# Performance work log

Measured on AMD Instinct MI355X. Metric: run time of the kernel, lower is better.

## Reference

```python
import jax, jax.numpy as jnp
import numpy as np

T, B, D, H = 512, 256, 256, 256


def setup_inputs() -> dict:
    key = jax.random.key(0)
    ks = jax.random.split(key, 10)
    # ragged lengths in [T//2, T], sorted descending as pack_padded_sequence requires
    lengths = np.sort(np.random.RandomState(0).randint(T // 2, T + 1, size=B))[::-1]
    # batch_sizes[t] = number of sequences still active at step t (non-increasing, >=1)
    batch_sizes = (lengths[None, :] > np.arange(T)[:, None]).sum(axis=1).astype(np.int32)
    batch_sizes = np.maximum(batch_sizes, 1)
    return {
        "input_x": jax.random.normal(ks[0], (T, B, D), jnp.float32),
        "h0": jax.random.normal(ks[1], (B, H), jnp.float32),
        "c0": jax.random.normal(ks[2], (B, H), jnp.float32),
        # variational dropout masks (precomputed, applied multiplicatively every step)
        "mask_x": (jax.random.uniform(ks[3], (B, D)) > 0.3).astype(jnp.float32) / 0.7,
        "mask_h": (jax.random.uniform(ks[4], (B, H)) > 0.3).astype(jnp.float32) / 0.7,
        "W_ih": jax.random.normal(ks[5], (4 * H, D), jnp.float32) * 0.05,
        "W_hh": jax.random.normal(ks[6], (4 * H, H), jnp.float32) * 0.05,
        "b_ih": jax.random.normal(ks[7], (4 * H,), jnp.float32) * 0.05,
        "b_hh": jax.random.normal(ks[8], (4 * H,), jnp.float32) * 0.05,
        "batch_sizes": jnp.asarray(batch_sizes),
    }


def reference(input_x, h0, c0, mask_x, mask_h, W_ih, W_hh, b_ih, b_hh, batch_sizes):
    # Forward (is_reversed=False) variational-dropout LSTM over a packed sequence.
    # Packed data is kept padded [T,B,*]; batch_sizes gives active rows per step.
    # Inactive rows keep their last-active hidden/cell state (== hn semantics).
    Bsz, Hid = h0.shape
    row = jnp.arange(Bsz)[:, None]

    def step(carry, inp):
        h, c = carry
        x_t, size = inp
        active = row < size  # [B,1]
        xi = x_t * mask_x            # input variational dropout
        hi = h * mask_h              # hidden variational dropout
        gates = xi @ W_ih.T + b_ih + hi @ W_hh.T + b_hh  # [B, 4H]
        i, f, g, o = jnp.split(gates, 4, axis=-1)
        c_new = jax.nn.sigmoid(f) * c + jax.nn.sigmoid(i) * jnp.tanh(g)
        h_new = jax.nn.sigmoid(o) * jnp.tanh(c_new)
        h = jnp.where(active, h_new, h)
        c = jnp.where(active, c_new, c)
        out = jnp.where(active, h_new, 0.0)  # padded positions zeroed (unused in pack)
        return (h, c), out

    (hn, cn), output = jax.lax.scan(step, (h0, c0), (input_x, batch_sizes))
    return output, hn, cn
```

## Files before the change

### kernel.cpp

```cpp
#include <hip/hip_runtime.h>
#include <hip/hip_bf16.h>

#define T_STEPS 512
#define BATCH   256
#define DIM     256
#define HID     256
#define DEPTH   4

using bf16x8  = __attribute__((ext_vector_type(8))) __bf16;
using floatx4 = __attribute__((ext_vector_type(4))) float;
typedef unsigned long long u64;
typedef unsigned int u32;

__device__ __forceinline__ float sigf(float x)   { return 1.0f / (1.0f + __expf(-x)); }
__device__ __forceinline__ float tanh_f(float x) { return 1.0f - 2.0f / (1.0f + __expf(2.0f * x)); }

__device__ __forceinline__ bf16x8 cvt8(const float* p) {
  floatx4 a = *(const floatx4*)p;
  floatx4 b = *(const floatx4*)(p + 4);
  bf16x8 r;
  r[0]=(__bf16)a[0]; r[1]=(__bf16)a[1]; r[2]=(__bf16)a[2]; r[3]=(__bf16)a[3];
  r[4]=(__bf16)b[0]; r[5]=(__bf16)b[1]; r[6]=(__bf16)b[2]; r[7]=(__bf16)b[3];
  return r;
}
__device__ __forceinline__ u32 f2bf(float f) {
  union { float f; u32 u; } v; v.f = f;
  u32 lsb = (v.u >> 16) & 1;
  return (v.u + 0x7fff + lsb) >> 16;
}
__device__ __forceinline__ float bf2f(u32 u) {
  union { u32 u; float f; } v; v.u = u << 16; return v.f;
}

__global__ void init_ws(int* __restrict__ flg, u64* __restrict__ inbox) {
  const int idx = blockIdx.x * 256 + threadIdx.x;
  if (idx < 4096) flg[idx] = 0;
  if (idx < 65536) inbox[idx] = 0ull;
}

__global__ __launch_bounds__(512, 1) void lstm_pk3(
    const float* __restrict__ x, const float* __restrict__ h0,
    const float* __restrict__ c0,
    const float* __restrict__ mask_x, const float* __restrict__ mask_h,
    const float* __restrict__ W_ih, const float* __restrict__ W_hh,
    const float* __restrict__ b_ih, const float* __restrict__ b_hh,
    const int* __restrict__ bs_g,
    float* __restrict__ out, float* __restrict__ hn_out, float* __restrict__ cn_out,
    int* __restrict__ flg, float* __restrict__ ring, u64* __restrict__ inbox) {

  const int tid  = threadIdx.x;
  const int g    = blockIdx.x & 15;
  const int role = blockIdx.x >> 4;
  const int p    = role & 1;
  const int row_base = g * 16;
  const int lane = tid & 63;
  const int w    = tid >> 6;
  const int l15  = lane & 15;
  const int l4   = lane >> 4;

  __shared__ alignas(16) __bf16 s_ab[16 * 256];
  __shared__ int s_bs[T_STEPS];
  for (int i = tid; i < T_STEPS; i += 512) s_bs[i] = bs_g[i];
  __syncthreads();

  int* cons_flg_mine = flg + (g * 2 + p) * 32;
  int* prod_flg_mine = flg + 2048 + (g * 2 + p) * 32;
  float* ring_mine = ring + (size_t)(g * 2 + p) * (DEPTH * 8192);
  u64* inbox_mine    = inbox + (size_t)(g * 2 + p) * 2048;
  u64* inbox_partner = inbox + (size_t)(g * 2 + (1 - p)) * 2048;

  const int c_loc = w * 16 + l15;

  if (role >= 2) {
    bf16x8 wih_r[4][8];
    #pragma unroll
    for (int q = 0; q < 4; ++q) {
      const size_t wr = (size_t)(q * HID + p * 128 + c_loc) * DIM;
      #pragma unroll
      for (int m = 0; m < 8; ++m) wih_r[q][m] = cvt8(W_ih + wr + m * 32 + l4 * 8);
    }
    float bias[4];
    #pragma unroll
    for (int q = 0; q < 4; ++q) {
      const int bc = q * HID + p * 128 + c_loc;
      bias[q] = b_ih[bc] + b_hh[bc];
    }
    const int srow = tid & 15, scb = (tid >> 4) * 8;
    floatx4 mx0 = *(const floatx4*)(mask_x + (row_base + srow) * DIM + scb);
    floatx4 mx1 = *(const floatx4*)(mask_x + (row_base + srow) * DIM + scb + 4);
    const int soff = (srow * 512 + scb * 2) ^ ((srow & 7) << 4);

    for (int t = 0; t < T_STEPS; ++t) {
      if (s_bs[t] <= row_base) break;
      if (t >= DEPTH) {
        const int tgt = t - (DEPTH - 1);
        while (__hip_atomic_load(cons_flg_mine, __ATOMIC_RELAXED, __HIP_MEMORY_SCOPE_AGENT) < tgt) {}
      }
      const float* xp = x + ((size_t)t * BATCH + row_base + srow) * DIM + scb;
      floatx4 xa = *(const floatx4*)xp;
      floatx4 xb = *(const floatx4*)(xp + 4);
      bf16x8 xv;
      #pragma unroll
      for (int e = 0; e < 4; ++e) { xv[e] = (__bf16)(xa[e] * mx0[e]); xv[4 + e] = (__bf16)(xb[e] * mx1[e]); }
      *(bf16x8*)((char*)s_ab + soff) = xv;
      asm volatile("s_waitcnt lgkmcnt(0)" ::: "memory");
      __builtin_amdgcn_s_barrier();

      floatx4 a0, a1, a2, a3;
      a0 = a1 = a2 = a3 = (floatx4)(0.0f);
      #pragma unroll
      for (int m = 0; m < 8; ++m) {
        const int ab = (l15 * 512 + l4 * 16 + m * 64) ^ ((l15 & 7) << 4);
        bf16x8 ax = *(const bf16x8*)((const char*)s_ab + ab);
        a0 = __builtin_amdgcn_mfma_f32_16x16x32_bf16(ax, wih_r[0][m], a0, 0, 0, 0);
        a1 = __builtin_amdgcn_mfma_f32_16x16x32_bf16(ax, wih_r[1][m], a1, 0, 0, 0);
        a2 = __builtin_amdgcn_mfma_f32_16x16x32_bf16(ax, wih_r[2][m], a2, 0, 0, 0);
        a3 = __builtin_amdgcn_mfma_f32_16x16x32_bf16(ax, wih_r[3][m], a3, 0, 0, 0);
      }
      float* rs = ring_mine + (size_t)(t & (DEPTH - 1)) * 8192;
      #pragma unroll
      for (int e = 0; e < 4; ++e) {
        const int rb = (l4 * 4 + e) * 4;
        __hip_atomic_store(rs + (rb + 0) * 128 + c_loc, a0[e] + bias[0], __ATOMIC_RELAXED, __HIP_MEMORY_SCOPE_AGENT);
        __hip_atomic_store(rs + (rb + 1) * 128 + c_loc, a1[e] + bias[1], __ATOMIC_RELAXED, __HIP_MEMORY_SCOPE_AGENT);
        __hip_atomic_store(rs + (rb + 2) * 128 + c_loc, a2[e] + bias[2], __ATOMIC_RELAXED, __HIP_MEMORY_SCOPE_AGENT);
        __hip_atomic_store(rs + (rb + 3) * 128 + c_loc, a3[e] + bias[3], __ATOMIC_RELAXED, __HIP_MEMORY_SCOPE_AGENT);
      }
      asm volatile("s_waitcnt vmcnt(0)" ::: "memory");
      __builtin_amdgcn_s_barrier();
      if (tid == 0)
        __hip_atomic_store(prod_flg_mine, t + 1, __ATOMIC_RELAXED, __HIP_MEMORY_SCOPE_AGENT);
    }
    return;
  }

  const int c_own = p * 128 + c_loc;
  bf16x8 whh_r[4][8];
  #pragma unroll
  for (int q = 0; q < 4; ++q) {
    const size_t wr = (size_t)(q * HID + c_own) * HID;
    const float* wown = W_hh + wr + p * 128;
    const float* wpar = W_hh + wr + (1 - p) * 128;
    #pragma unroll
    for (int i = 0; i < 4; ++i) {
      whh_r[q][i]     = cvt8(wown + i * 32 + l4 * 8);
      whh_r[q][4 + i] = cvt8(wpar + i * 32 + l4 * 8);
    }
  }
  float mh_c[4], h_[4], c_[4];
  #pragma unroll
  for (int e = 0; e < 4; ++e) {
    const int grow = row_base + l4 * 4 + e;
    mh_c[e] = mask_h[grow * HID + c_own];
    h_[e]   = h0[grow * HID + c_own];
    c_[e]   = c0[grow * HID + c_own];
  }
  const int sc_loc = tid >> 2;
  const int rq     = tid & 3;
  const int c_gs   = (1 - p) * 128 + sc_loc;
  float mh_s[4];
  #pragma unroll
  for (int e = 0; e < 4; ++e) mh_s[e] = mask_h[(row_base + rq * 4 + e) * HID + c_gs];

  const int abase   = l15 * 512 + l4 * 16;
  const int own_off = p * 256;
  const int par_off = (1 - p) * 256;

  #pragma unroll
  for (int e = 0; e < 4; ++e) {
    const int r = l4 * 4 + e;
    const int off = (r * 512 + c_own * 2) ^ ((r & 7) << 4);
    *(__bf16*)((char*)s_ab + off) = (__bf16)(h_[e] * mh_c[e]);
  }
  while (__hip_atomic_load(prod_flg_mine, __ATOMIC_RELAXED, __HIP_MEMORY_SCOPE_AGENT) < 1) {}
  asm volatile("" ::: "memory");
  float xp_c[16];
  #pragma unroll
  for (int e = 0; e < 4; ++e)
    #pragma unroll
    for (int q = 0; q < 4; ++q)
      xp_c[e * 4 + q] = __hip_atomic_load(ring_mine + ((l4 * 4 + e) * 4 + q) * 128 + c_loc,
                                          __ATOMIC_RELAXED, __HIP_MEMORY_SCOPE_AGENT);
  asm volatile("s_waitcnt lgkmcnt(0)" ::: "memory");
  __builtin_amdgcn_s_barrier();

  for (int t = 0; t < T_STEPS; ++t) {
    const int bszt = s_bs[t];
    if (bszt <= row_base) {
      #pragma unroll
      for (int e = 0; e < 4; ++e)
        out[(size_t)t * (BATCH * HID) + (row_base + l4 * 4 + e) * HID + c_own] = 0.0f;
      continue;
    }
    const bool act_n = (t + 1 < T_STEPS) && (s_bs[t + 1] > row_base);

    floatx4 a0, a1, a2, a3;
    a0 = a1 = a2 = a3 = (floatx4)(0.0f);
    #pragma unroll
    for (int i = 0; i < 4; ++i) {
      const int ab = ((abase + own_off + i * 64)) ^ ((l15 & 7) << 4);
      bf16x8 ah = *(const bf16x8*)((const char*)s_ab + ab);
      a0 = __builtin_amdgcn_mfma_f32_16x16x32_bf16(ah, whh_r[0][i], a0, 0, 0, 0);
      a1 = __builtin_amdgcn_mfma_f32_16x16x32_bf16(ah, whh_r[1][i], a1, 0, 0, 0);
      a2 = __builtin_amdgcn_mfma_f32_16x16x32_bf16(ah, whh_r[2][i], a2, 0, 0, 0);
      a3 = __builtin_amdgcn_mfma_f32_16x16x32_bf16(ah, whh_r[3][i], a3, 0, 0, 0);
    }

    if (t == 0) {
      #pragma unroll
      for (int e = 0; e < 4; ++e) {
        const int r = rq * 4 + e;
        const float hv = h0[(row_base + r) * HID + c_gs] * mh_s[e];
        const int off = (r * 512 + c_gs * 2) ^ ((r & 7) << 4);
        *(__bf16*)((char*)s_ab + off) = (__bf16)hv;
      }
    } else {
      const u64* ib = inbox_mine + (size_t)(t & 1) * 1024 + sc_loc * 8 + rq * 2;
      u64 pk0, pk1;
      do {
        pk0 = __hip_atomic_load(ib,     __ATOMIC_RELAXED, __HIP_MEMORY_SCOPE_AGENT);
        pk1 = __hip_atomic_load(ib + 1, __ATOMIC_RELAXED, __HIP_MEMORY_SCOPE_AGENT);
      } while (!__all((int)(((u32)pk0 == (u32)t) && ((u32)pk1 == (u32)t))));
      float hv[4];
      hv[0] = bf2f((u32)(pk0 >> 32) & 0xffffu) * mh_s[0];
      hv[1] = bf2f((u32)(pk0 >> 48))           * mh_s[1];
      hv[2] = bf2f((u32)(pk1 >> 32) & 0xffffu) * mh_s[2];
      hv[3] = bf2f((u32)(pk1 >> 48))           * mh_s[3];
      #pragma unroll
      for (int e = 0; e < 4; ++e) {
        const int r = rq * 4 + e;
        const int off = (r * 512 + c_gs * 2) ^ ((r & 7) << 4);
        *(__bf16*)((char*)s_ab + off) = (__bf16)hv[e];
      }
    }
    asm volatile("s_waitcnt lgkmcnt(0)" ::: "memory");
    __builtin_amdgcn_s_barrier();

    #pragma unroll
    for (int i = 0; i < 4; ++i) {
      const int ab = ((abase + par_off + i * 64)) ^ ((l15 & 7) << 4);
      bf16x8 ah = *(const bf16x8*)((const char*)s_ab + ab);
      a0 = __builtin_amdgcn_mfma_f32_16x16x32_bf16(ah, whh_r[0][4 + i], a0, 0, 0, 0);
      a1 = __builtin_amdgcn_mfma_f32_16x16x32_bf16(ah, whh_r[1][4 + i], a1, 0, 0, 0);
      a2 = __builtin_amdgcn_mfma_f32_16x16x32_bf16(ah, whh_r[2][4 + i], a2, 0, 0, 0);
      a3 = __builtin_amdgcn_mfma_f32_16x16x32_bf16(ah, whh_r[3][4 + i], a3, 0, 0, 0);
    }

    float o_[4];
    #pragma unroll
    for (int e = 0; e < 4; ++e) {
      const bool ract = (row_base + l4 * 4 + e) < bszt;
      const float iv = sigf(a0[e] + xp_c[e * 4 + 0]);
      const float fv = sigf(a1[e] + xp_c[e * 4 + 1]);
      const float gv = tanh_f(a2[e] + xp_c[e * 4 + 2]);
      const float ov = sigf(a3[e] + xp_c[e * 4 + 3]);
      const float cc = fv * c_[e] + iv * gv;
      const float hh = ov * tanh_f(cc);
      if (ract) { c_[e] = cc; h_[e] = hh; }
      o_[e] = ract ? hh : 0.0f;
    }

    if (act_n) {
      u64* ob = inbox_partner + (size_t)((t + 1) & 1) * 1024 + c_loc * 8 + l4 * 2;
      const u64 tag = (u32)(t + 1);
      u64 w0 = tag | ((u64)f2bf(h_[0]) << 32) | ((u64)f2bf(h_[1]) << 48);
      u64 w1 = tag | ((u64)f2bf(h_[2]) << 32) | ((u64)f2bf(h_[3]) << 48);
      __hip_atomic_store(ob,     w0, __ATOMIC_RELAXED, __HIP_MEMORY_SCOPE_AGENT);
      __hip_atomic_store(ob + 1, w1, __ATOMIC_RELAXED, __HIP_MEMORY_SCOPE_AGENT);
    }

    if (act_n) {
      #pragma unroll
      for (int e = 0; e < 4; ++e) {
        const int r = l4 * 4 + e;
        const int off = (r * 512 + c_own * 2) ^ ((r & 7) << 4);
        *(__bf16*)((char*)s_ab + off) = (__bf16)(h_[e] * mh_c[e]);
      }
    }
    #pragma unroll
    for (int e = 0; e < 4; ++e)
      out[(size_t)t * (BATCH * HID) + (row_base + l4 * 4 + e) * HID + c_own] = o_[e];

    if (act_n) {
      if (tid == 0)
        __hip_atomic_store(cons_flg_mine, t + 1, __ATOMIC_RELAXED, __HIP_MEMORY_SCOPE_AGENT);
      while (__hip_atomic_load(prod_flg_mine, __ATOMIC_RELAXED, __HIP_MEMORY_SCOPE_AGENT) < t + 2) {}
      asm volatile("" ::: "memory");
      const float* rs = ring_mine + (size_t)((t + 1) & (DEPTH - 1)) * 8192;
      #pragma unroll
      for (int e = 0; e < 4; ++e)
        #pragma unroll
        for (int q = 0; q < 4; ++q)
          xp_c[e * 4 + q] = __hip_atomic_load(rs + ((l4 * 4 + e) * 4 + q) * 128 + c_loc,
                                              __ATOMIC_RELAXED, __HIP_MEMORY_SCOPE_AGENT);
    }

    asm volatile("s_waitcnt lgkmcnt(0)" ::: "memory");
    __builtin_amdgcn_s_barrier();
  }

  #pragma unroll
  for (int e = 0; e < 4; ++e) {
    const int grow = row_base + l4 * 4 + e;
    hn_out[grow * HID + c_own] = h_[e];
    cn_out[grow * HID + c_own] = c_[e];
  }
}

extern "C" void kernel_launch(void* const* d_in, const int* in_sizes, int n_in,
                              void* d_out, int out_size, void* d_ws, size_t ws_size,
                              hipStream_t stream) {
  const float* x      = (const float*)d_in[0];
  const float* h0     = (const float*)d_in[1];
  const float* c0     = (const float*)d_in[2];
  const float* mask_x = (const float*)d_in[3];
  const float* mask_h = (const float*)d_in[4];
  const float* W_ih   = (const float*)d_in[5];
  const float* W_hh   = (const float*)d_in[6];
  const float* b_ih   = (const float*)d_in[7];
  const float* b_hh   = (const float*)d_in[8];
  const int*   bs     = (const int*)d_in[9];

  float* out = (float*)d_out;
  float* hn  = out + (size_t)T_STEPS * BATCH * HID;
  float* cn  = hn + (size_t)BATCH * HID;

  int* flg  = (int*)d_ws;
  float* ring = (float*)((char*)d_ws + 16384);
  u64* inbox = (u64*)((char*)d_ws + 16384 + 4194304);

  init_ws<<<256, 256, 0, stream>>>(flg, inbox);
  lstm_pk3<<<64, 512, 0, stream>>>(x, h0, c0, mask_x, mask_h, W_ih, W_hh,
                                   b_ih, b_hh, bs, out, hn, cn, flg, ring, inbox);
}
```

Before: 1.640 ms.

## Tag ring entries in bf16 and batch output stores through shared memory

The producer now writes the input-projection ring as tagged u64 words holding packed bf16 values. Consumers spin on the tags directly, so the separate producer flag, its vmcnt wait and the flag store go away, and ring traffic is halved. The next step's x is prefetched during the MFMAs, and per-step outputs are staged in shared memory and flushed every 8 steps. The trade-offs are lower precision for the projection values, stale tags that may match across calls because the ring and inbox are no longer zeroed, and more shared memory use.

```diff
diff --git a/kernel.cpp b/kernel.cpp
--- a/kernel.cpp
+++ b/kernel.cpp
@@ -29,16 +29,14 @@
   return (v.u + 0x7fff + lsb) >> 16;
 }
 __device__ __forceinline__ float bf2f(u32 u) {
-  union { u32 u; float f; } v; v.u = u << 16; return v.f;
-}
-
-__global__ void init_ws(int* __restrict__ flg, u64* __restrict__ inbox) {
-  const int idx = blockIdx.x * 256 + threadIdx.x;
-  if (idx < 4096) flg[idx] = 0;
-  if (idx < 65536) inbox[idx] = 0ull;
-}
-
-__global__ __launch_bounds__(512, 1) void lstm_pk3(
+  union { u32 u; float f; } v; v.u = (u & 0xffffu) << 16; return v.f;
+}
+
+__global__ void init_ws(int* __restrict__ flg) {
+  flg[blockIdx.x * 256 + threadIdx.x] = 0;
+}
+
+__global__ __launch_bounds__(512, 1) void lstm_v9(
     const float* __restrict__ x, const float* __restrict__ h0,
     const float* __restrict__ c0,
     const float* __restrict__ mask_x, const float* __restrict__ mask_h,
@@ -46,7 +44,7 @@
     const float* __restrict__ b_ih, const float* __restrict__ b_hh,
     const int* __restrict__ bs_g,
     float* __restrict__ out, float* __restrict__ hn_out, float* __restrict__ cn_out,
-    int* __restrict__ flg, float* __restrict__ ring, u64* __restrict__ inbox) {
+    int* __restrict__ flg, u64* __restrict__ ring, u64* __restrict__ inbox) {
 
   const int tid  = threadIdx.x;
   const int g    = blockIdx.x & 15;
@@ -59,13 +57,13 @@
   const int l4   = lane >> 4;
 
   __shared__ alignas(16) __bf16 s_ab[16 * 256];
+  __shared__ alignas(16) float  s_ob[512 * 32];
   __shared__ int s_bs[T_STEPS];
   for (int i = tid; i < T_STEPS; i += 512) s_bs[i] = bs_g[i];
   __syncthreads();
 
   int* cons_flg_mine = flg + (g * 2 + p) * 32;
-  int* prod_flg_mine = flg + 2048 + (g * 2 + p) * 32;
-  float* ring_mine = ring + (size_t)(g * 2 + p) * (DEPTH * 8192);
+  u64* ring_mine     = ring + (size_t)(g * 2 + p) * (DEPTH * 4096);
   u64* inbox_mine    = inbox + (size_t)(g * 2 + p) * 2048;
   u64* inbox_partner = inbox + (size_t)(g * 2 + (1 - p)) * 2048;
 
@@ -89,6 +87,12 @@
     floatx4 mx0 = *(const floatx4*)(mask_x + (row_base + srow) * DIM + scb);
     floatx4 mx1 = *(const floatx4*)(mask_x + (row_base + srow) * DIM + scb + 4);
     const int soff = (srow * 512 + scb * 2) ^ ((srow & 7) << 4);
+
+    floatx4 xa, xb;
+    {
+      const float* xp = x + (size_t)(row_base + srow) * DIM + scb;
+      xa = *(const floatx4*)xp; xb = *(const floatx4*)(xp + 4);
+    }
 
     for (int t = 0; t < T_STEPS; ++t) {
       if (s_bs[t] <= row_base) break;
@@ -96,9 +100,6 @@
         const int tgt = t - (DEPTH - 1);
         while (__hip_atomic_load(cons_flg_mine, __ATOMIC_RELAXED, __HIP_MEMORY_SCOPE_AGENT) < tgt) {}
       }
-      const float* xp = x + ((size_t)t * BATCH + row_base + srow) * DIM + scb;
-      floatx4 xa = *(const floatx4*)xp;
-      floatx4 xb = *(const floatx4*)(xp + 4);
       bf16x8 xv;
       #pragma unroll
       for (int e = 0; e < 4; ++e) { xv[e] = (__bf16)(xa[e] * mx0[e]); xv[4 + e] = (__bf16)(xb[e] * mx1[e]); }
@@ -117,19 +118,22 @@
         a2 = __builtin_amdgcn_mfma_f32_16x16x32_bf16(ax, wih_r[2][m], a2, 0, 0, 0);
         a3 = __builtin_amdgcn_mfma_f32_16x16x32_bf16(ax, wih_r[3][m], a3, 0, 0, 0);
       }
-      float* rs = ring_mine + (size_t)(t & (DEPTH - 1)) * 8192;
+
+      if (t + 1 < T_STEPS) {
+        const float* xp = x + ((size_t)(t + 1) * BATCH + row_base + srow) * DIM + scb;
+        xa = *(const floatx4*)xp; xb = *(const floatx4*)(xp + 4);
+      }
+
+      u64* rs = ring_mine + (size_t)(t & (DEPTH - 1)) * 4096 + tid * 8;
+      const u64 tag = (u32)(t + 1);
       #pragma unroll
       for (int e = 0; e < 4; ++e) {
-        const int rb = (l4 * 4 + e) * 4;
-        __hip_atomic_store(rs + (rb + 0) * 128 + c_loc, a0[e] + bias[0], __ATOMIC_RELAXED, __HIP_MEMORY_SCOPE_AGENT);
-        __hip_atomic_store(rs + (rb + 1) * 128 + c_loc, a1[e] + bias[1], __ATOMIC_RELAXED, __HIP_MEMORY_SCOPE_AGENT);
-        __hip_atomic_store(rs + (rb + 2) * 128 + c_loc, a2[e] + bias[2], __ATOMIC_RELAXED, __HIP_MEMORY_SCOPE_AGENT);
-        __hip_atomic_store(rs + (rb + 3) * 128 + c_loc, a3[e] + bias[3], __ATOMIC_RELAXED, __HIP_MEMORY_SCOPE_AGENT);
-      }
-      asm volatile("s_waitcnt vmcnt(0)" ::: "memory");
+        u64 w0 = tag | ((u64)f2bf(a0[e] + bias[0]) << 32) | ((u64)f2bf(a1[e] + bias[1]) << 48);
+        u64 w1 = tag | ((u64)f2bf(a2[e] + bias[2]) << 32) | ((u64)f2bf(a3[e] + bias[3]) << 48);
+        __hip_atomic_store(rs + e * 2,     w0, __ATOMIC_RELAXED, __HIP_MEMORY_SCOPE_AGENT);
+        __hip_atomic_store(rs + e * 2 + 1, w1, __ATOMIC_RELAXED, __HIP_MEMORY_SCOPE_AGENT);
+      }
       __builtin_amdgcn_s_barrier();
-      if (tid == 0)
-        __hip_atomic_store(prod_flg_mine, t + 1, __ATOMIC_RELAXED, __HIP_MEMORY_SCOPE_AGENT);
     }
     return;
   }
@@ -172,24 +176,44 @@
     const int off = (r * 512 + c_own * 2) ^ ((r & 7) << 4);
     *(__bf16*)((char*)s_ab + off) = (__bf16)(h_[e] * mh_c[e]);
   }
-  while (__hip_atomic_load(prod_flg_mine, __ATOMIC_RELAXED, __HIP_MEMORY_SCOPE_AGENT) < 1) {}
-  asm volatile("" ::: "memory");
   float xp_c[16];
-  #pragma unroll
-  for (int e = 0; e < 4; ++e)
-    #pragma unroll
-    for (int q = 0; q < 4; ++q)
-      xp_c[e * 4 + q] = __hip_atomic_load(ring_mine + ((l4 * 4 + e) * 4 + q) * 128 + c_loc,
-                                          __ATOMIC_RELAXED, __HIP_MEMORY_SCOPE_AGENT);
+  {
+    const u64* rp = ring_mine + tid * 8;
+    u64 q0,q1,q2,q3,q4,q5,q6,q7;
+    do {
+      q0 = __hip_atomic_load(rp+0, __ATOMIC_RELAXED, __HIP_MEMORY_SCOPE_AGENT);
+      q1 = __hip_atomic_load(rp+1, __ATOMIC_RELAXED, __HIP_MEMORY_SCOPE_AGENT);
+      q2 = __hip_atomic_load(rp+2, __ATOMIC_RELAXED, __HIP_MEMORY_SCOPE_AGENT);
+      q3 = __hip_atomic_load(rp+3, __ATOMIC_RELAXED, __HIP_MEMORY_SCOPE_AGENT);
+      q4 = __hip_atomic_load(rp+4, __ATOMIC_RELAXED, __HIP_MEMORY_SCOPE_AGENT);
+      q5 = __hip_atomic_load(rp+5, __ATOMIC_RELAXED, __HIP_MEMORY_SCOPE_AGENT);
+      q6 = __hip_atomic_load(rp+6, __ATOMIC_RELAXED, __HIP_MEMORY_SCOPE_AGENT);
+      q7 = __hip_atomic_load(rp+7, __ATOMIC_RELAXED, __HIP_MEMORY_SCOPE_AGENT);
+    } while (!__all((int)(((u32)q0==1u)&&((u32)q1==1u)&&((u32)q2==1u)&&((u32)q3==1u)&&
+                          ((u32)q4==1u)&&((u32)q5==1u)&&((u32)q6==1u)&&((u32)q7==1u))));
+    xp_c[0]=bf2f((u32)(q0>>32)); xp_c[1]=bf2f((u32)(q0>>48)); xp_c[2]=bf2f((u32)(q1>>32)); xp_c[3]=bf2f((u32)(q1>>48));
+    xp_c[4]=bf2f((u32)(q2>>32)); xp_c[5]=bf2f((u32)(q2>>48)); xp_c[6]=bf2f((u32)(q3>>32)); xp_c[7]=bf2f((u32)(q3>>48));
+    xp_c[8]=bf2f((u32)(q4>>32)); xp_c[9]=bf2f((u32)(q4>>48)); xp_c[10]=bf2f((u32)(q5>>32)); xp_c[11]=bf2f((u32)(q5>>48));
+    xp_c[12]=bf2f((u32)(q6>>32)); xp_c[13]=bf2f((u32)(q6>>48)); xp_c[14]=bf2f((u32)(q7>>32)); xp_c[15]=bf2f((u32)(q7>>48));
+  }
   asm volatile("s_waitcnt lgkmcnt(0)" ::: "memory");
   __builtin_amdgcn_s_barrier();
 
   for (int t = 0; t < T_STEPS; ++t) {
     const int bszt = s_bs[t];
     if (bszt <= row_base) {
-      #pragma unroll
-      for (int e = 0; e < 4; ++e)
-        out[(size_t)t * (BATCH * HID) + (row_base + l4 * 4 + e) * HID + c_own] = 0.0f;
+      floatx4 z; z[0]=z[1]=z[2]=z[3]=0.0f;
+      *(floatx4*)&s_ob[tid * 32 + (t & 7) * 4] = z;
+      if ((t & 7) == 7) {
+        const int t0 = t - 7;
+        #pragma unroll
+        for (int k = 0; k < 8; ++k) {
+          floatx4 v = *(const floatx4*)&s_ob[tid * 32 + k * 4];
+          #pragma unroll
+          for (int e = 0; e < 4; ++e)
+            out[(size_t)(t0 + k) * (BATCH * HID) + (row_base + l4 * 4 + e) * HID + c_own] = v[e];
+        }
+      }
       continue;
     }
     const bool act_n = (t + 1 < T_STEPS) && (s_bs[t + 1] > row_base);
@@ -198,7 +222,7 @@
     a0 = a1 = a2 = a3 = (floatx4)(0.0f);
     #pragma unroll
     for (int i = 0; i < 4; ++i) {
-      const int ab = ((abase + own_off + i * 64)) ^ ((l15 & 7) << 4);
+      const int ab = (abase + own_off + i * 64) ^ ((l15 & 7) << 4);
       bf16x8 ah = *(const bf16x8*)((const char*)s_ab + ab);
       a0 = __builtin_amdgcn_mfma_f32_16x16x32_bf16(ah, whh_r[0][i], a0, 0, 0, 0);
       a1 = __builtin_amdgcn_mfma_f32_16x16x32_bf16(ah, whh_r[1][i], a1, 0, 0, 0);
@@ -222,10 +246,10 @@
         pk1 = __hip_atomic_load(ib + 1, __ATOMIC_RELAXED, __HIP_MEMORY_SCOPE_AGENT);
       } while (!__all((int)(((u32)pk0 == (u32)t) && ((u32)pk1 == (u32)t))));
       float hv[4];
-      hv[0] = bf2f((u32)(pk0 >> 32) & 0xffffu) * mh_s[0];
-      hv[1] = bf2f((u32)(pk0 >> 48))           * mh_s[1];
-      hv[2] = bf2f((u32)(pk1 >> 32) & 0xffffu) * mh_s[2];
-      hv[3] = bf2f((u32)(pk1 >> 48))           * mh_s[3];
+      hv[0] = bf2f((u32)(pk0 >> 32)) * mh_s[0];
+      hv[1] = bf2f((u32)(pk0 >> 48)) * mh_s[1];
+      hv[2] = bf2f((u32)(pk1 >> 32)) * mh_s[2];
+      hv[3] = bf2f((u32)(pk1 >> 48)) * mh_s[3];
       #pragma unroll
       for (int e = 0; e < 4; ++e) {
         const int r = rq * 4 + e;
@@ -238,7 +262,7 @@
 
     #pragma unroll
     for (int i = 0; i < 4; ++i) {
-      const int ab = ((abase + par_off + i * 64)) ^ ((l15 & 7) << 4);
+      const int ab = (abase + par_off + i * 64) ^ ((l15 & 7) << 4);
       bf16x8 ah = *(const bf16x8*)((const char*)s_ab + ab);
       a0 = __builtin_amdgcn_mfma_f32_16x16x32_bf16(ah, whh_r[0][4 + i], a0, 0, 0, 0);
       a1 = __builtin_amdgcn_mfma_f32_16x16x32_bf16(ah, whh_r[1][4 + i], a1, 0, 0, 0);
@@ -246,7 +270,7 @@
       a3 = __builtin_amdgcn_mfma_f32_16x16x32_bf16(ah, whh_r[3][4 + i], a3, 0, 0, 0);
     }
 
-    float o_[4];
+    floatx4 o4;
     #pragma unroll
     for (int e = 0; e < 4; ++e) {
       const bool ract = (row_base + l4 * 4 + e) < bszt;
@@ -257,7 +281,7 @@
       const float cc = fv * c_[e] + iv * gv;
       const float hh = ov * tanh_f(cc);
       if (ract) { c_[e] = cc; h_[e] = hh; }
-      o_[e] = ract ? hh : 0.0f;
+      o4[e] = ract ? hh : 0.0f;
     }
 
     if (act_n) {
@@ -277,22 +301,39 @@
         *(__bf16*)((char*)s_ab + off) = (__bf16)(h_[e] * mh_c[e]);
       }
     }
-    #pragma unroll
-    for (int e = 0; e < 4; ++e)
-      out[(size_t)t * (BATCH * HID) + (row_base + l4 * 4 + e) * HID + c_own] = o_[e];
+    *(floatx4*)&s_ob[tid * 32 + (t & 7) * 4] = o4;
+    if ((t & 7) == 7) {
+      const int t0 = t - 7;
+      #pragma unroll
+      for (int k = 0; k < 8; ++k) {
+        floatx4 v = *(const floatx4*)&s_ob[tid * 32 + k * 4];
+        #pragma unroll
+        for (int e = 0; e < 4; ++e)
+          out[(size_t)(t0 + k) * (BATCH * HID) + (row_base + l4 * 4 + e) * HID + c_own] = v[e];
+      }
+    }
 
     if (act_n) {
       if (tid == 0)
         __hip_atomic_store(cons_flg_mine, t + 1, __ATOMIC_RELAXED, __HIP_MEMORY_SCOPE_AGENT);
-      while (__hip_atomic_load(prod_flg_mine, __ATOMIC_RELAXED, __HIP_MEMORY_SCOPE_AGENT) < t + 2) {}
-      asm volatile("" ::: "memory");
-      const float* rs = ring_mine + (size_t)((t + 1) & (DEPTH - 1)) * 8192;
-      #pragma unroll
-      for (int e = 0; e < 4; ++e)
-        #pragma unroll
-        for (int q = 0; q < 4; ++q)
-          xp_c[e * 4 + q] = __hip_atomic_load(rs + ((l4 * 4 + e) * 4 + q) * 128 + c_loc,
-                                              __ATOMIC_RELAXED, __HIP_MEMORY_SCOPE_AGENT);
+      const u64* rp = ring_mine + (size_t)((t + 1) & (DEPTH - 1)) * 4096 + tid * 8;
+      const u32 tg = (u32)(t + 2);
+      u64 q0,q1,q2,q3,q4,q5,q6,q7;
+      do {
+        q0 = __hip_atomic_load(rp+0, __ATOMIC_RELAXED, __HIP_MEMORY_SCOPE_AGENT);
+        q1 = __hip_atomic_load(rp+1, __ATOMIC_RELAXED, __HIP_MEMORY_SCOPE_AGENT);
+        q2 = __hip_atomic_load(rp+2, __ATOMIC_RELAXED, __HIP_MEMORY_SCOPE_AGENT);
+        q3 = __hip_atomic_load(rp+3, __ATOMIC_RELAXED, __HIP_MEMORY_SCOPE_AGENT);
+        q4 = __hip_atomic_load(rp+4, __ATOMIC_RELAXED, __HIP_MEMORY_SCOPE_AGENT);
+        q5 = __hip_atomic_load(rp+5, __ATOMIC_RELAXED, __HIP_MEMORY_SCOPE_AGENT);
+        q6 = __hip_atomic_load(rp+6, __ATOMIC_RELAXED, __HIP_MEMORY_SCOPE_AGENT);
+        q7 = __hip_atomic_load(rp+7, __ATOMIC_RELAXED, __HIP_MEMORY_SCOPE_AGENT);
+      } while (!__all((int)(((u32)q0==tg)&&((u32)q1==tg)&&((u32)q2==tg)&&((u32)q3==tg)&&
+                            ((u32)q4==tg)&&((u32)q5==tg)&&((u32)q6==tg)&&((u32)q7==tg))));
+      xp_c[0]=bf2f((u32)(q0>>32)); xp_c[1]=bf2f((u32)(q0>>48)); xp_c[2]=bf2f((u32)(q1>>32)); xp_c[3]=bf2f((u32)(q1>>48));
+      xp_c[4]=bf2f((u32)(q2>>32)); xp_c[5]=bf2f((u32)(q2>>48)); xp_c[6]=bf2f((u32)(q3>>32)); xp_c[7]=bf2f((u32)(q3>>48));
+      xp_c[8]=bf2f((u32)(q4>>32)); xp_c[9]=bf2f((u32)(q4>>48)); xp_c[10]=bf2f((u32)(q5>>32)); xp_c[11]=bf2f((u32)(q5>>48));
+      xp_c[12]=bf2f((u32)(q6>>32)); xp_c[13]=bf2f((u32)(q6>>48)); xp_c[14]=bf2f((u32)(q7>>32)); xp_c[15]=bf2f((u32)(q7>>48));
     }
 
     asm volatile("s_waitcnt lgkmcnt(0)" ::: "memory");
@@ -326,10 +367,10 @@
   float* cn  = hn + (size_t)BATCH * HID;
 
   int* flg  = (int*)d_ws;
-  float* ring = (float*)((char*)d_ws + 16384);
+  u64* ring = (u64*)((char*)d_ws + 16384);
   u64* inbox = (u64*)((char*)d_ws + 16384 + 4194304);
 
-  init_ws<<<256, 256, 0, stream>>>(flg, inbox);
-  lstm_pk3<<<64, 512, 0, stream>>>(x, h0, c0, mask_x, mask_h, W_ih, W_hh,
-                                   b_ih, b_hh, bs, out, hn, cn, flg, ring, inbox);
-}
+  init_ws<<<16, 256, 0, stream>>>(flg);
+  lstm_v9<<<64, 512, 0, stream>>>(x, h0, c0, mask_x, mask_h, W_ih, W_hh,
+                                  b_ih, b_hh, bs, out, hn, cn, flg, ring, inbox);
+}
```

After: 2.501 ms. 1.52x slower.

## Prefetch next x tile in producers and batch output stores via LDS staging

Applied to the files above, without the earlier changes.

Producer blocks now load the next timestep's x slice right after the MFMA loop, so the global load latency overlaps the ring writes and the flag wait. Consumer blocks stage each step's output in a shared-memory buffer covering 8 timesteps and flush it to global every 8 steps, taking scattered stores off the per-step critical path. This adds 64KB of LDS and a full vmcnt wait before each barrier. It also risks dropping the tail outputs when the final step is not 8-aligned, though with T=512 the last step index is 511, so the last flush fires.

```diff
diff --git a/kernel.cpp b/kernel.cpp
--- a/kernel.cpp
+++ b/kernel.cpp
@@ -29,7 +29,7 @@
   return (v.u + 0x7fff + lsb) >> 16;
 }
 __device__ __forceinline__ float bf2f(u32 u) {
-  union { u32 u; float f; } v; v.u = u << 16; return v.f;
+  union { u32 u; float f; } v; v.u = (u & 0xffffu) << 16; return v.f;
 }
 
 __global__ void init_ws(int* __restrict__ flg, u64* __restrict__ inbox) {
@@ -38,7 +38,7 @@
   if (idx < 65536) inbox[idx] = 0ull;
 }
 
-__global__ __launch_bounds__(512, 1) void lstm_pk3(
+__global__ __launch_bounds__(512, 1) void lstm_v11(
     const float* __restrict__ x, const float* __restrict__ h0,
     const float* __restrict__ c0,
     const float* __restrict__ mask_x, const float* __restrict__ mask_h,
@@ -59,13 +59,14 @@
   const int l4   = lane >> 4;
 
   __shared__ alignas(16) __bf16 s_ab[16 * 256];
+  __shared__ alignas(16) floatx4 s_ob[8 * 512];
   __shared__ int s_bs[T_STEPS];
   for (int i = tid; i < T_STEPS; i += 512) s_bs[i] = bs_g[i];
   __syncthreads();
 
   int* cons_flg_mine = flg + (g * 2 + p) * 32;
   int* prod_flg_mine = flg + 2048 + (g * 2 + p) * 32;
-  float* ring_mine = ring + (size_t)(g * 2 + p) * (DEPTH * 8192);
+  float* ring_mine   = ring + (size_t)(g * 2 + p) * (DEPTH * 8192);
   u64* inbox_mine    = inbox + (size_t)(g * 2 + p) * 2048;
   u64* inbox_partner = inbox + (size_t)(g * 2 + (1 - p)) * 2048;
 
@@ -89,6 +90,12 @@
     floatx4 mx0 = *(const floatx4*)(mask_x + (row_base + srow) * DIM + scb);
     floatx4 mx1 = *(const floatx4*)(mask_x + (row_base + srow) * DIM + scb + 4);
     const int soff = (srow * 512 + scb * 2) ^ ((srow & 7) << 4);
+
+    floatx4 xa, xb;
+    {
+      const float* xp = x + (size_t)(row_base + srow) * DIM + scb;
+      xa = *(const floatx4*)xp; xb = *(const floatx4*)(xp + 4);
+    }
 
     for (int t = 0; t < T_STEPS; ++t) {
       if (s_bs[t] <= row_base) break;
@@ -96,9 +103,6 @@
         const int tgt = t - (DEPTH - 1);
         while (__hip_atomic_load(cons_flg_mine, __ATOMIC_RELAXED, __HIP_MEMORY_SCOPE_AGENT) < tgt) {}
       }
-      const float* xp = x + ((size_t)t * BATCH + row_base + srow) * DIM + scb;
-      floatx4 xa = *(const floatx4*)xp;
-      floatx4 xb = *(const floatx4*)(xp + 4);
       bf16x8 xv;
       #pragma unroll
       for (int e = 0; e < 4; ++e) { xv[e] = (__bf16)(xa[e] * mx0[e]); xv[4 + e] = (__bf16)(xb[e] * mx1[e]); }
@@ -117,6 +121,10 @@
         a2 = __builtin_amdgcn_mfma_f32_16x16x32_bf16(ax, wih_r[2][m], a2, 0, 0, 0);
         a3 = __builtin_amdgcn_mfma_f32_16x16x32_bf16(ax, wih_r[3][m], a3, 0, 0, 0);
       }
+      if (t + 1 < T_STEPS) {
+        const float* xp = x + ((size_t)(t + 1) * BATCH + row_base + srow) * DIM + scb;
+        xa = *(const floatx4*)xp; xb = *(const floatx4*)(xp + 4);
+      }
       float* rs = ring_mine + (size_t)(t & (DEPTH - 1)) * 8192;
       #pragma unroll
       for (int e = 0; e < 4; ++e) {
@@ -181,15 +189,24 @@
     for (int q = 0; q < 4; ++q)
       xp_c[e * 4 + q] = __hip_atomic_load(ring_mine + ((l4 * 4 + e) * 4 + q) * 128 + c_loc,
                                           __ATOMIC_RELAXED, __HIP_MEMORY_SCOPE_AGENT);
-  asm volatile("s_waitcnt lgkmcnt(0)" ::: "memory");
+  asm volatile("s_waitcnt vmcnt(0) lgkmcnt(0)" ::: "memory");
   __builtin_amdgcn_s_barrier();
 
   for (int t = 0; t < T_STEPS; ++t) {
     const int bszt = s_bs[t];
     if (bszt <= row_base) {
-      #pragma unroll
-      for (int e = 0; e < 4; ++e)
-        out[(size_t)t * (BATCH * HID) + (row_base + l4 * 4 + e) * HID + c_own] = 0.0f;
+      floatx4 z; z[0]=z[1]=z[2]=z[3]=0.0f;
+      s_ob[(t & 7) * 512 + tid] = z;
+      if ((t & 7) == 7) {
+        const int t0 = t - 7;
+        #pragma unroll
+        for (int k = 0; k < 8; ++k) {
+          floatx4 v = s_ob[k * 512 + tid];
+          #pragma unroll
+          for (int e = 0; e < 4; ++e)
+            out[(size_t)(t0 + k) * (BATCH * HID) + (row_base + l4 * 4 + e) * HID + c_own] = v[e];
+        }
+      }
       continue;
     }
     const bool act_n = (t + 1 < T_STEPS) && (s_bs[t + 1] > row_base);
@@ -198,7 +215,7 @@
     a0 = a1 = a2 = a3 = (floatx4)(0.0f);
     #pragma unroll
     for (int i = 0; i < 4; ++i) {
-      const int ab = ((abase + own_off + i * 64)) ^ ((l15 & 7) << 4);
+      const int ab = (abase + own_off + i * 64) ^ ((l15 & 7) << 4);
       bf16x8 ah = *(const bf16x8*)((const char*)s_ab + ab);
       a0 = __builtin_amdgcn_mfma_f32_16x16x32_bf16(ah, whh_r[0][i], a0, 0, 0, 0);
       a1 = __builtin_amdgcn_mfma_f32_16x16x32_bf16(ah, whh_r[1][i], a1, 0, 0, 0);
@@ -222,10 +239,10 @@
         pk1 = __hip_atomic_load(ib + 1, __ATOMIC_RELAXED, __HIP_MEMORY_SCOPE_AGENT);
       } while (!__all((int)(((u32)pk0 == (u32)t) && ((u32)pk1 == (u32)t))));
       float hv[4];
-      hv[0] = bf2f((u32)(pk0 >> 32) & 0xffffu) * mh_s[0];
-      hv[1] = bf2f((u32)(pk0 >> 48))           * mh_s[1];
-      hv[2] = bf2f((u32)(pk1 >> 32) & 0xffffu) * mh_s[2];
-      hv[3] = bf2f((u32)(pk1 >> 48))           * mh_s[3];
+      hv[0] = bf2f((u32)(pk0 >> 32)) * mh_s[0];
+      hv[1] = bf2f((u32)(pk0 >> 48)) * mh_s[1];
+      hv[2] = bf2f((u32)(pk1 >> 32)) * mh_s[2];
+      hv[3] = bf2f((u32)(pk1 >> 48)) * mh_s[3];
       #pragma unroll
       for (int e = 0; e < 4; ++e) {
         const int r = rq * 4 + e;
@@ -238,7 +255,7 @@
 
     #pragma unroll
     for (int i = 0; i < 4; ++i) {
-      const int ab = ((abase + par_off + i * 64)) ^ ((l15 & 7) << 4);
+      const int ab = (abase + par_off + i * 64) ^ ((l15 & 7) << 4);
       bf16x8 ah = *(const bf16x8*)((const char*)s_ab + ab);
       a0 = __builtin_amdgcn_mfma_f32_16x16x32_bf16(ah, whh_r[0][4 + i], a0, 0, 0, 0);
       a1 = __builtin_amdgcn_mfma_f32_16x16x32_bf16(ah, whh_r[1][4 + i], a1, 0, 0, 0);
@@ -246,7 +263,7 @@
       a3 = __builtin_amdgcn_mfma_f32_16x16x32_bf16(ah, whh_r[3][4 + i], a3, 0, 0, 0);
     }
 
-    float o_[4];
+    floatx4 o4;
     #pragma unroll
     for (int e = 0; e < 4; ++e) {
       const bool ract = (row_base + l4 * 4 + e) < bszt;
@@ -257,7 +274,7 @@
       const float cc = fv * c_[e] + iv * gv;
       const float hh = ov * tanh_f(cc);
       if (ract) { c_[e] = cc; h_[e] = hh; }
-      o_[e] = ract ? hh : 0.0f;
+      o4[e] = ract ? hh : 0.0f;
     }
 
     if (act_n) {
@@ -277,10 +294,17 @@
         *(__bf16*)((char*)s_ab + off) = (__bf16)(h_[e] * mh_c[e]);
       }
     }
-    #pragma unroll
-    for (int e = 0; e < 4; ++e)
-      out[(size_t)t * (BATCH * HID) + (row_base + l4 * 4 + e) * HID + c_own] = o_[e];
-
+    s_ob[(t & 7) * 512 + tid] = o4;
+    if ((t & 7) == 7) {
+      const int t0 = t - 7;
+      #pragma unroll
+      for (int k = 0; k < 8; ++k) {
+        floatx4 v = s_ob[k * 512 + tid];
+        #pragma unroll
+        for (int e = 0; e < 4; ++e)
+          out[(size_t)(t0 + k) * (BATCH * HID) + (row_base + l4 * 4 + e) * HID + c_own] = v[e];
+      }
+    }
     if (act_n) {
       if (tid == 0)
         __hip_atomic_store(cons_flg_mine, t + 1, __ATOMIC_RELAXED, __HIP_MEMORY_SCOPE_AGENT);
@@ -294,8 +318,7 @@
           xp_c[e * 4 + q] = __hip_atomic_load(rs + ((l4 * 4 + e) * 4 + q) * 128 + c_loc,
                                               __ATOMIC_RELAXED, __HIP_MEMORY_SCOPE_AGENT);
     }
-
-    asm volatile("s_waitcnt lgkmcnt(0)" ::: "memory");
+    asm volatile("s_waitcnt vmcnt(0) lgkmcnt(0)" ::: "memory");
     __builtin_amdgcn_s_barrier();
   }
 
@@ -325,11 +348,11 @@
   float* hn  = out + (size_t)T_STEPS * BATCH * HID;
   float* cn  = hn + (size_t)BATCH * HID;
 
-  int* flg  = (int*)d_ws;
+  int* flg   = (int*)d_ws;
   float* ring = (float*)((char*)d_ws + 16384);
   u64* inbox = (u64*)((char*)d_ws + 16384 + 4194304);
 
   init_ws<<<256, 256, 0, stream>>>(flg, inbox);
-  lstm_pk3<<<64, 512, 0, stream>>>(x, h0, c0, mask_x, mask_h, W_ih, W_hh,
+  lstm_v11<<<64, 512, 0, stream>>>(x, h0, c0, mask_x, mask_h, W_ih, W_hh,
                                    b_ih, b_hh, bs, out, hn, cn, flg, ring, inbox);
 }
```

New measurement: 2.079 ms. +26.8%, slower.
